# Kernel optimization log

Hardware: AMD Instinct MI355X
Metric: run time of the kernel (lower is better)

## Reference

```python
import jax, jax.numpy as jnp
import numpy as np

SCALES = [3, 5, 7, 9]


def _conv1d(x, w, b, k):
    # x: (BN, 1, L), w: (1, 1, k), b: (1,) -> (BN, 1, L), 'same' padding (k//2)
    y = jax.lax.conv_general_dilated(
        x, w, window_strides=(1,), padding=[(k // 2, k // 2)],
        dimension_numbers=("NCH", "OIH", "NCH"))
    return y + b[None, :, None]


def setup_inputs() -> dict:
    key = jax.random.key(0)
    ks = jax.random.split(key, 16)
    B, N, L = 64, 321, 720
    inp = {"x": jax.random.normal(ks[0], (B, N, L), dtype=jnp.float32)}
    # Conv1d(1,1,k) params, kaiming-ish scale 1/sqrt(k)
    for i, s in enumerate(SCALES):
        inp[f"cw{i}"] = jax.random.normal(ks[1 + 2 * i], (1, 1, s), dtype=jnp.float32) / np.sqrt(s)
        inp[f"cb{i}"] = jax.random.normal(ks[2 + 2 * i], (1,), dtype=jnp.float32) * 0.01
    # weight_net: Linear(4,32) -> ReLU -> Linear(32,4) -> Softmax
    inp["W1"] = jax.random.normal(ks[10], (4, 32), dtype=jnp.float32) / np.sqrt(4.0)
    inp["b1"] = jnp.zeros((32,), dtype=jnp.float32)
    inp["W2"] = jax.random.normal(ks[11], (32, 4), dtype=jnp.float32) / np.sqrt(32.0)
    inp["b2"] = jnp.zeros((4,), dtype=jnp.float32)
    return inp


def reference(x, cw0, cb0, cw1, cb1, cw2, cb2, cw3, cb3, W1, b1, W2, b2):
    B, N, L = x.shape
    xf = x.reshape(B * N, 1, L)
    cparams = [(cw0, cb0), (cw1, cb1), (cw2, cb2), (cw3, cb3)]
    feats, ents = [], []
    for (w, b), k in zip(cparams, SCALES):
        f = _conv1d(xf, w, b, k)                      # (BN, 1, L)
        prob = jax.nn.softmax(f, axis=-1)
        ent = -(prob * jnp.log(prob + 1e-8)).sum(axis=-1)  # (BN, 1)
        feats.append(f)
        ents.append(ent)
    entropy_vec = jnp.concatenate(ents, axis=-1)      # (BN, 4)
    h = jax.nn.relu(entropy_vec @ W1 + b1)
    weights = jax.nn.softmax(h @ W2 + b2, axis=-1)    # (BN, 4)
    stacked = jnp.stack(feats, axis=1)                # (BN, 4, 1, L)
    trend = (stacked * weights[:, :, None, None]).sum(axis=1)  # (BN, 1, L)
    return trend.reshape(B, N, L)
```

## Files before the change

kernel.cpp:

```cpp
#include <hip/hip_runtime.h>
#include <math.h>

#define NT 64
#define L_LEN 720
#define NROWS (64 * 321)

#define LOG2E 1.4426950408889634f
#define LN2   0.6931471805599453f

typedef float f32x2 __attribute__((ext_vector_type(2)));

__device__ __forceinline__ f32x2 pkfma(f32x2 a, f32x2 b, f32x2 c) {
    return __builtin_elementwise_fma(a, b, c);
}

template<int CTRL, int RM>
__device__ __forceinline__ float dpp_add(float x) {
    int t = __builtin_amdgcn_update_dpp(0, __float_as_int(x), CTRL, RM, 0xf, true);
    return x + __int_as_float(t);
}

__device__ __forceinline__ float wave_sum64(float x) {
    x = dpp_add<0x111, 0xf>(x);
    x = dpp_add<0x112, 0xf>(x);
    x = dpp_add<0x114, 0xf>(x);
    x = dpp_add<0x118, 0xf>(x);
    x = dpp_add<0x142, 0xa>(x);
    x = dpp_add<0x143, 0xc>(x);
    return __int_as_float(__builtin_amdgcn_readlane(__float_as_int(x), 63));
}

__device__ __forceinline__ float half_sum32(float x) {
    x = dpp_add<0x111, 0xf>(x);
    x = dpp_add<0x112, 0xf>(x);
    x = dpp_add<0x114, 0xf>(x);
    x = dpp_add<0x118, 0xf>(x);
    x = dpp_add<0x142, 0xa>(x);
    return __int_as_float(__builtin_amdgcn_readlane(__float_as_int(x), 31));
}

__global__ __launch_bounds__(NT, 4) void trend_kernel(
    const float* __restrict__ x,
    const float* __restrict__ cw0, const float* __restrict__ cb0,
    const float* __restrict__ cw1, const float* __restrict__ cb1,
    const float* __restrict__ cw2, const float* __restrict__ cb2,
    const float* __restrict__ cw3, const float* __restrict__ cb3,
    const float* __restrict__ W1, const float* __restrict__ b1,
    const float* __restrict__ W2, const float* __restrict__ b2,
    float* __restrict__ out)
{
    const int lane = threadIdx.x;
    const int row  = blockIdx.x;

    const float* __restrict__ xr = x + (size_t)row * L_LEN;

    const int ll = (lane < 60) ? lane : 59;
    const int e0 = 12 * ll - 4;
    float xw[20];
#pragma unroll
    for (int q = 0; q < 5; ++q) {
        int e = e0 + 4 * q;
        e = (e < 0) ? 0 : ((e > L_LEN - 4) ? (L_LEN - 4) : e);
        float4 v = *(const float4*)(xr + e);
        xw[4 * q + 0] = v.x; xw[4 * q + 1] = v.y;
        xw[4 * q + 2] = v.z; xw[4 * q + 3] = v.w;
    }

    const int hidx = lane & 31;
    float w1r[4];
#pragma unroll
    for (int s = 0; s < 4; ++s) w1r[s] = W1[s * 32 + hidx];
    const float b1r = b1[hidx];
    const float4 w2v = ((const float4*)W2)[hidx];
    const float b20 = b2[0], b21 = b2[1], b22 = b2[2], b23 = b2[3];

    const float* cws[4] = {cw0, cw1, cw2, cw3};
    const float* cbs[4] = {cb0, cb1, cb2, cb3};
    float w[4][9], bs[4];
#pragma unroll
    for (int s = 0; s < 4; ++s) {
        const int k = 3 + 2 * s;
        bs[s] = cbs[s][0];
#pragma unroll
        for (int t = 0; t < 9; ++t)
            w[s][t] = (t < k) ? cws[s][t] : 0.0f;
    }

    if (lane == 0)  { xw[0] = 0.f; xw[1] = 0.f; xw[2] = 0.f; xw[3] = 0.f; }
    if (lane == 59) { xw[16] = 0.f; xw[17] = 0.f; xw[18] = 0.f; xw[19] = 0.f; }

#pragma unroll
    for (int t = 0; t < 20; ++t) asm volatile("" : "+v"(xw[t]));

    f32x2 p[14];
#pragma unroll
    for (int i = 0; i < 14; ++i) p[i] = (f32x2){xw[i], xw[i + 6]};

    const f32x2 l2e = (f32x2){LOG2E, LOG2E};
    f32x2 fu[4][6];
    f32x2 Spk[4] = {{0.f,0.f},{0.f,0.f},{0.f,0.f},{0.f,0.f}};
    f32x2 Tpk[4] = {{0.f,0.f},{0.f,0.f},{0.f,0.f},{0.f,0.f}};
#pragma unroll
    for (int j = 0; j < 6; ++j) {
#pragma unroll
        for (int s = 0; s < 4; ++s) {
            const int k = 3 + 2 * s;
            const int off = 3 - s;
            f32x2 f = (f32x2){bs[s], bs[s]};
#pragma unroll
            for (int t = 0; t < k; ++t) {
                const f32x2 wv = (f32x2){w[s][t], w[s][t]};
                f = pkfma(wv, p[j + off + t], f);
            }
            fu[s][j] = f;
            f32x2 u = f * l2e;
            f32x2 ev;
            ev.x = __builtin_amdgcn_exp2f(u.x);
            ev.y = __builtin_amdgcn_exp2f(u.y);
            Spk[s] += ev;
            Tpk[s] = pkfma(f, ev, Tpk[s]);
        }
    }

#pragma unroll
    for (int s = 0; s < 4; ++s)
#pragma unroll
        for (int j = 0; j < 6; ++j) {
            asm volatile("" : "+v"(fu[s][j].x));
            asm volatile("" : "+v"(fu[s][j].y));
        }

    const bool active = lane < 60;
    float S[4], Tn[4];
#pragma unroll
    for (int s = 0; s < 4; ++s) {
        S[s]  = active ? (Spk[s].x + Spk[s].y) : 0.0f;
        Tn[s] = active ? (Tpk[s].x + Tpk[s].y) : 0.0f;
    }

    float ent[4];
#pragma unroll
    for (int s = 0; s < 4; ++s) {
        float Sg = wave_sum64(S[s]);
        float Tg = wave_sum64(Tn[s]);
        ent[s] = fmaf(LN2, __builtin_amdgcn_logf(Sg),
                      -Tg * __builtin_amdgcn_rcpf(Sg));
    }

    float h = b1r;
#pragma unroll
    for (int s = 0; s < 4; ++s) h = fmaf(ent[s], w1r[s], h);
    h = fmaxf(h, 0.0f);

    float lg0 = half_sum32(h * w2v.x) + b20;
    float lg1 = half_sum32(h * w2v.y) + b21;
    float lg2 = half_sum32(h * w2v.z) + b22;
    float lg3 = half_sum32(h * w2v.w) + b23;

    float m = fmaxf(fmaxf(lg0, lg1), fmaxf(lg2, lg3));
    float e0w = __expf(lg0 - m), e1w = __expf(lg1 - m);
    float e2w = __expf(lg2 - m), e3w = __expf(lg3 - m);
    float inv = 1.0f / (e0w + e1w + e2w + e3w);
    const float wg0 = e0w * inv, wg1 = e1w * inv;
    const float wg2 = e2w * inv, wg3 = e3w * inv;

    if (active) {
        f32x2 o[6];
#pragma unroll
        for (int j = 0; j < 6; ++j) {
            f32x2 acc = (f32x2){wg0, wg0} * fu[0][j];
            acc = pkfma((f32x2){wg1, wg1}, fu[1][j], acc);
            acc = pkfma((f32x2){wg2, wg2}, fu[2][j], acc);
            acc = pkfma((f32x2){wg3, wg3}, fu[3][j], acc);
            o[j] = acc;
        }
        float* __restrict__ orow = out + (size_t)row * L_LEN + 12 * lane;
        float4 v0 = {o[0].x, o[1].x, o[2].x, o[3].x};
        float4 v1 = {o[4].x, o[5].x, o[0].y, o[1].y};
        float4 v2 = {o[2].y, o[3].y, o[4].y, o[5].y};
        *(float4*)(orow)     = v0;
        *(float4*)(orow + 4) = v1;
        *(float4*)(orow + 8) = v2;
    }
}

extern "C" void kernel_launch(void* const* d_in, const int* in_sizes, int n_in,
                              void* d_out, int out_size, void* d_ws, size_t ws_size,
                              hipStream_t stream) {
    const float* xp  = (const float*)d_in[0];
    const float* cw0 = (const float*)d_in[1];
    const float* cb0 = (const float*)d_in[2];
    const float* cw1 = (const float*)d_in[3];
    const float* cb1 = (const float*)d_in[4];
    const float* cw2 = (const float*)d_in[5];
    const float* cb2 = (const float*)d_in[6];
    const float* cw3 = (const float*)d_in[7];
    const float* cb3 = (const float*)d_in[8];
    const float* W1  = (const float*)d_in[9];
    const float* b1  = (const float*)d_in[10];
    const float* W2  = (const float*)d_in[11];
    const float* b2  = (const float*)d_in[12];
    float* outp = (float*)d_out;

    trend_kernel<<<NROWS, NT, 0, stream>>>(xp, cw0, cb0, cw1, cb1, cw2, cb2,
                                           cw3, cb3, W1, b1, W2, b2, outp);
}
```

Measured before the change: 33.03 us.

## Assign strided float4 chunks per lane for coalesced loads and stores

Instead of each lane owning 12 contiguous elements, each lane now owns three float4 chunks spaced 60 chunks apart, and loads each chunk together with its neighbours for the halo. Consecutive lanes then touch consecutive 16-byte chunks, which makes the global loads and stores fully coalesced, in place of the previous 48-byte per-lane stride. The cost is more redundant halo loads (9 float4 per lane instead of 5) and a change in how packed pairs are formed from even and odd offsets.

```diff
diff --git a/kernel.cpp b/kernel.cpp
--- a/kernel.cpp
+++ b/kernel.cpp
@@ -3,6 +3,7 @@
 
 #define NT 64
 #define L_LEN 720
+#define NCHUNKS 180
 #define NROWS (64 * 321)
 
 #define LOG2E 1.4426950408889634f
@@ -52,18 +53,21 @@
     const int lane = threadIdx.x;
     const int row  = blockIdx.x;
 
-    const float* __restrict__ xr = x + (size_t)row * L_LEN;
-
-    const int ll = (lane < 60) ? lane : 59;
-    const int e0 = 12 * ll - 4;
-    float xw[20];
-#pragma unroll
-    for (int q = 0; q < 5; ++q) {
-        int e = e0 + 4 * q;
-        e = (e < 0) ? 0 : ((e > L_LEN - 4) ? (L_LEN - 4) : e);
-        float4 v = *(const float4*)(xr + e);
-        xw[4 * q + 0] = v.x; xw[4 * q + 1] = v.y;
-        xw[4 * q + 2] = v.z; xw[4 * q + 3] = v.w;
+    const float*  __restrict__ xr = x + (size_t)row * L_LEN;
+    const float4* __restrict__ xc = (const float4*)xr;
+
+    const int  ll     = (lane < 60) ? lane : 59;
+    const bool active = lane < 60;
+
+    float4 xq[3][3];
+#pragma unroll
+    for (int q = 0; q < 3; ++q) {
+#pragma unroll
+        for (int r = 0; r < 3; ++r) {
+            int c = ll + 60 * q + r - 1;
+            c = (c < 0) ? 0 : ((c > NCHUNKS - 1) ? (NCHUNKS - 1) : c);
+            xq[q][r] = xc[c];
+        }
     }
 
     const int hidx = lane & 31;
@@ -86,51 +90,65 @@
             w[s][t] = (t < k) ? cws[s][t] : 0.0f;
     }
 
-    if (lane == 0)  { xw[0] = 0.f; xw[1] = 0.f; xw[2] = 0.f; xw[3] = 0.f; }
-    if (lane == 59) { xw[16] = 0.f; xw[17] = 0.f; xw[18] = 0.f; xw[19] = 0.f; }
-
-#pragma unroll
-    for (int t = 0; t < 20; ++t) asm volatile("" : "+v"(xw[t]));
-
-    f32x2 p[14];
-#pragma unroll
-    for (int i = 0; i < 14; ++i) p[i] = (f32x2){xw[i], xw[i + 6]};
+    if (lane == 0)  xq[0][0] = (float4){0.f, 0.f, 0.f, 0.f};
+    if (lane == 59) xq[2][2] = (float4){0.f, 0.f, 0.f, 0.f};
+
+#pragma unroll
+    for (int q = 0; q < 3; ++q)
+#pragma unroll
+        for (int r = 0; r < 3; ++r)
+            asm volatile("" : "+v"(xq[q][r].x), "+v"(xq[q][r].y),
+                              "+v"(xq[q][r].z), "+v"(xq[q][r].w));
 
     const f32x2 l2e = (f32x2){LOG2E, LOG2E};
     f32x2 fu[4][6];
     f32x2 Spk[4] = {{0.f,0.f},{0.f,0.f},{0.f,0.f},{0.f,0.f}};
     f32x2 Tpk[4] = {{0.f,0.f},{0.f,0.f},{0.f,0.f},{0.f,0.f}};
-#pragma unroll
-    for (int j = 0; j < 6; ++j) {
-#pragma unroll
-        for (int s = 0; s < 4; ++s) {
-            const int k = 3 + 2 * s;
-            const int off = 3 - s;
-            f32x2 f = (f32x2){bs[s], bs[s]};
-#pragma unroll
-            for (int t = 0; t < k; ++t) {
-                const f32x2 wv = (f32x2){w[s][t], w[s][t]};
-                f = pkfma(wv, p[j + off + t], f);
+
+#pragma unroll
+    for (int q = 0; q < 3; ++q) {
+        const float xv[12] = {
+            xq[q][0].x, xq[q][0].y, xq[q][0].z, xq[q][0].w,
+            xq[q][1].x, xq[q][1].y, xq[q][1].z, xq[q][1].w,
+            xq[q][2].x, xq[q][2].y, xq[q][2].z, xq[q][2].w };
+
+        f32x2 pe[6], po[5];
+#pragma unroll
+        for (int i = 0; i < 6; ++i) pe[i] = (f32x2){xv[2 * i], xv[2 * i + 1]};
+#pragma unroll
+        for (int i = 0; i < 5; ++i) po[i] = (f32x2){xv[2 * i + 1], xv[2 * i + 2]};
+
+#pragma unroll
+        for (int pi = 0; pi < 2; ++pi) {
+            const int j0 = 2 * pi;
+#pragma unroll
+            for (int s = 0; s < 4; ++s) {
+                const int k = 3 + 2 * s;
+                const int off = 3 - s;
+                f32x2 f = (f32x2){bs[s], bs[s]};
+#pragma unroll
+                for (int t = 0; t < k; ++t) {
+                    const int i = j0 + off + t;
+                    const f32x2 pv = (i & 1) ? po[i >> 1] : pe[i >> 1];
+                    f = pkfma((f32x2){w[s][t], w[s][t]}, pv, f);
+                }
+                fu[s][2 * q + pi] = f;
+                f32x2 u = f * l2e;
+                f32x2 ev;
+                ev.x = __builtin_amdgcn_exp2f(u.x);
+                ev.y = __builtin_amdgcn_exp2f(u.y);
+                Spk[s] += ev;
+                Tpk[s] = pkfma(f, ev, Tpk[s]);
             }
-            fu[s][j] = f;
-            f32x2 u = f * l2e;
-            f32x2 ev;
-            ev.x = __builtin_amdgcn_exp2f(u.x);
-            ev.y = __builtin_amdgcn_exp2f(u.y);
-            Spk[s] += ev;
-            Tpk[s] = pkfma(f, ev, Tpk[s]);
         }
     }
 
 #pragma unroll
     for (int s = 0; s < 4; ++s)
 #pragma unroll
-        for (int j = 0; j < 6; ++j) {
-            asm volatile("" : "+v"(fu[s][j].x));
-            asm volatile("" : "+v"(fu[s][j].y));
-        }
-
-    const bool active = lane < 60;
+        for (int j = 0; j < 6; ++j)
+            asm volatile("" : "+v"(fu[s][j].x), "+v"(fu[s][j].y));
+
     float S[4], Tn[4];
 #pragma unroll
     for (int s = 0; s < 4; ++s) {
@@ -165,22 +183,20 @@
     const float wg2 = e2w * inv, wg3 = e3w * inv;
 
     if (active) {
-        f32x2 o[6];
-#pragma unroll
-        for (int j = 0; j < 6; ++j) {
-            f32x2 acc = (f32x2){wg0, wg0} * fu[0][j];
-            acc = pkfma((f32x2){wg1, wg1}, fu[1][j], acc);
-            acc = pkfma((f32x2){wg2, wg2}, fu[2][j], acc);
-            acc = pkfma((f32x2){wg3, wg3}, fu[3][j], acc);
-            o[j] = acc;
+        float4* __restrict__ oc = (float4*)(out + (size_t)row * L_LEN);
+#pragma unroll
+        for (int q = 0; q < 3; ++q) {
+            f32x2 o0 = (f32x2){wg0, wg0} * fu[0][2 * q];
+            o0 = pkfma((f32x2){wg1, wg1}, fu[1][2 * q], o0);
+            o0 = pkfma((f32x2){wg2, wg2}, fu[2][2 * q], o0);
+            o0 = pkfma((f32x2){wg3, wg3}, fu[3][2 * q], o0);
+            f32x2 o1 = (f32x2){wg0, wg0} * fu[0][2 * q + 1];
+            o1 = pkfma((f32x2){wg1, wg1}, fu[1][2 * q + 1], o1);
+            o1 = pkfma((f32x2){wg2, wg2}, fu[2][2 * q + 1], o1);
+            o1 = pkfma((f32x2){wg3, wg3}, fu[3][2 * q + 1], o1);
+            float4 v = {o0.x, o0.y, o1.x, o1.y};
+            oc[lane + 60 * q] = v;
         }
-        float* __restrict__ orow = out + (size_t)row * L_LEN + 12 * lane;
-        float4 v0 = {o[0].x, o[1].x, o[2].x, o[3].x};
-        float4 v1 = {o[4].x, o[5].x, o[0].y, o[1].y};
-        float4 v2 = {o[2].y, o[3].y, o[4].y, o[5].y};
-        *(float4*)(orow)     = v0;
-        *(float4*)(orow + 4) = v1;
-        *(float4*)(orow + 8) = v2;
     }
 }
 
```

Result: no change. 33.15 us (+0.4%).

## Process two rows per wave and recompute output via merged conv weights

Applied to the files above, without the earlier changes.

Each 64-thread block now handles two rows, loading both inputs up front and interleaving their convolution, entropy and reduction chains for more ILP and fewer blocks. Instead of keeping all four conv outputs live in registers until the mixing weights are known, the kernel folds the softmax weights into a single merged 9-tap filter and bias and recomputes the output from the input window. This cuts register pressure from stored features but adds an extra 9-tap pass and doubles per-thread state for two rows, which may still raise register use.

```diff
diff --git a/kernel.cpp b/kernel.cpp
--- a/kernel.cpp
+++ b/kernel.cpp
@@ -50,20 +50,25 @@
     float* __restrict__ out)
 {
     const int lane = threadIdx.x;
-    const int row  = blockIdx.x;
-
-    const float* __restrict__ xr = x + (size_t)row * L_LEN;
+    const int rowA = blockIdx.x * 2;
+    const int rowB = rowA + 1;
+
+    const float* __restrict__ xa = x + (size_t)rowA * L_LEN;
+    const float* __restrict__ xb = x + (size_t)rowB * L_LEN;
 
     const int ll = (lane < 60) ? lane : 59;
     const int e0 = 12 * ll - 4;
-    float xw[20];
+    float xwA[20], xwB[20];
 #pragma unroll
     for (int q = 0; q < 5; ++q) {
         int e = e0 + 4 * q;
         e = (e < 0) ? 0 : ((e > L_LEN - 4) ? (L_LEN - 4) : e);
-        float4 v = *(const float4*)(xr + e);
-        xw[4 * q + 0] = v.x; xw[4 * q + 1] = v.y;
-        xw[4 * q + 2] = v.z; xw[4 * q + 3] = v.w;
+        float4 va = *(const float4*)(xa + e);
+        float4 vb = *(const float4*)(xb + e);
+        xwA[4 * q + 0] = va.x; xwA[4 * q + 1] = va.y;
+        xwA[4 * q + 2] = va.z; xwA[4 * q + 3] = va.w;
+        xwB[4 * q + 0] = vb.x; xwB[4 * q + 1] = vb.y;
+        xwB[4 * q + 2] = vb.z; xwB[4 * q + 3] = vb.w;
     }
 
     const int hidx = lane & 31;
@@ -86,101 +91,149 @@
             w[s][t] = (t < k) ? cws[s][t] : 0.0f;
     }
 
-    if (lane == 0)  { xw[0] = 0.f; xw[1] = 0.f; xw[2] = 0.f; xw[3] = 0.f; }
-    if (lane == 59) { xw[16] = 0.f; xw[17] = 0.f; xw[18] = 0.f; xw[19] = 0.f; }
-
-#pragma unroll
-    for (int t = 0; t < 20; ++t) asm volatile("" : "+v"(xw[t]));
-
-    f32x2 p[14];
-#pragma unroll
-    for (int i = 0; i < 14; ++i) p[i] = (f32x2){xw[i], xw[i + 6]};
+    if (lane == 0) {
+#pragma unroll
+        for (int t = 0; t < 4; ++t) { xwA[t] = 0.f; xwB[t] = 0.f; }
+    }
+    if (lane == 59) {
+#pragma unroll
+        for (int t = 16; t < 20; ++t) { xwA[t] = 0.f; xwB[t] = 0.f; }
+    }
+
+    f32x2 pA[14], pB[14];
+#pragma unroll
+    for (int i = 0; i < 14; ++i) {
+        pA[i] = (f32x2){xwA[i], xwA[i + 6]};
+        pB[i] = (f32x2){xwB[i], xwB[i + 6]};
+    }
+#pragma unroll
+    for (int i = 0; i < 14; ++i) {
+        asm volatile("" : "+v"(pA[i].x), "+v"(pA[i].y));
+        asm volatile("" : "+v"(pB[i].x), "+v"(pB[i].y));
+    }
 
     const f32x2 l2e = (f32x2){LOG2E, LOG2E};
-    f32x2 fu[4][6];
-    f32x2 Spk[4] = {{0.f,0.f},{0.f,0.f},{0.f,0.f},{0.f,0.f}};
-    f32x2 Tpk[4] = {{0.f,0.f},{0.f,0.f},{0.f,0.f},{0.f,0.f}};
+    f32x2 SpkA[4] = {{0,0},{0,0},{0,0},{0,0}}, SpkB[4] = {{0,0},{0,0},{0,0},{0,0}};
+    f32x2 TpkA[4] = {{0,0},{0,0},{0,0},{0,0}}, TpkB[4] = {{0,0},{0,0},{0,0},{0,0}};
 #pragma unroll
     for (int j = 0; j < 6; ++j) {
 #pragma unroll
         for (int s = 0; s < 4; ++s) {
             const int k = 3 + 2 * s;
             const int off = 3 - s;
-            f32x2 f = (f32x2){bs[s], bs[s]};
+            f32x2 fA = (f32x2){bs[s], bs[s]};
+            f32x2 fB = fA;
 #pragma unroll
             for (int t = 0; t < k; ++t) {
                 const f32x2 wv = (f32x2){w[s][t], w[s][t]};
-                f = pkfma(wv, p[j + off + t], f);
+                fA = pkfma(wv, pA[j + off + t], fA);
+                fB = pkfma(wv, pB[j + off + t], fB);
             }
-            fu[s][j] = f;
-            f32x2 u = f * l2e;
-            f32x2 ev;
-            ev.x = __builtin_amdgcn_exp2f(u.x);
-            ev.y = __builtin_amdgcn_exp2f(u.y);
-            Spk[s] += ev;
-            Tpk[s] = pkfma(f, ev, Tpk[s]);
+            f32x2 uA = fA * l2e, uB = fB * l2e;
+            f32x2 eA, eB;
+            eA.x = __builtin_amdgcn_exp2f(uA.x);
+            eA.y = __builtin_amdgcn_exp2f(uA.y);
+            eB.x = __builtin_amdgcn_exp2f(uB.x);
+            eB.y = __builtin_amdgcn_exp2f(uB.y);
+            SpkA[s] += eA;                SpkB[s] += eB;
+            TpkA[s] = pkfma(fA, eA, TpkA[s]);
+            TpkB[s] = pkfma(fB, eB, TpkB[s]);
         }
     }
 
-#pragma unroll
-    for (int s = 0; s < 4; ++s)
+    const bool active = lane < 60;
+    float SA[4], TA[4], SB[4], TB[4];
+#pragma unroll
+    for (int s = 0; s < 4; ++s) {
+        SA[s] = active ? (SpkA[s].x + SpkA[s].y) : 0.0f;
+        TA[s] = active ? (TpkA[s].x + TpkA[s].y) : 0.0f;
+        SB[s] = active ? (SpkB[s].x + SpkB[s].y) : 0.0f;
+        TB[s] = active ? (TpkB[s].x + TpkB[s].y) : 0.0f;
+    }
+
+    float entA[4], entB[4];
+#pragma unroll
+    for (int s = 0; s < 4; ++s) {
+        float SgA = wave_sum64(SA[s]);
+        float TgA = wave_sum64(TA[s]);
+        float SgB = wave_sum64(SB[s]);
+        float TgB = wave_sum64(TB[s]);
+        entA[s] = fmaf(LN2, __builtin_amdgcn_logf(SgA),
+                       -TgA * __builtin_amdgcn_rcpf(SgA));
+        entB[s] = fmaf(LN2, __builtin_amdgcn_logf(SgB),
+                       -TgB * __builtin_amdgcn_rcpf(SgB));
+    }
+
+    float hA = b1r, hB = b1r;
+#pragma unroll
+    for (int s = 0; s < 4; ++s) {
+        hA = fmaf(entA[s], w1r[s], hA);
+        hB = fmaf(entB[s], w1r[s], hB);
+    }
+    hA = fmaxf(hA, 0.0f); hB = fmaxf(hB, 0.0f);
+
+    float lgA0 = half_sum32(hA * w2v.x) + b20;
+    float lgA1 = half_sum32(hA * w2v.y) + b21;
+    float lgA2 = half_sum32(hA * w2v.z) + b22;
+    float lgA3 = half_sum32(hA * w2v.w) + b23;
+    float lgB0 = half_sum32(hB * w2v.x) + b20;
+    float lgB1 = half_sum32(hB * w2v.y) + b21;
+    float lgB2 = half_sum32(hB * w2v.z) + b22;
+    float lgB3 = half_sum32(hB * w2v.w) + b23;
+
+    float mA = fmaxf(fmaxf(lgA0, lgA1), fmaxf(lgA2, lgA3));
+    float mB = fmaxf(fmaxf(lgB0, lgB1), fmaxf(lgB2, lgB3));
+    float eA0 = __expf(lgA0 - mA), eA1 = __expf(lgA1 - mA);
+    float eA2 = __expf(lgA2 - mA), eA3 = __expf(lgA3 - mA);
+    float eB0 = __expf(lgB0 - mB), eB1 = __expf(lgB1 - mB);
+    float eB2 = __expf(lgB2 - mB), eB3 = __expf(lgB3 - mB);
+    float invA = 1.0f / (eA0 + eA1 + eA2 + eA3);
+    float invB = 1.0f / (eB0 + eB1 + eB2 + eB3);
+    const float wgtA[4] = {eA0 * invA, eA1 * invA, eA2 * invA, eA3 * invA};
+    const float wgtB[4] = {eB0 * invB, eB1 * invB, eB2 * invB, eB3 * invB};
+
+    float WmA[9] = {0,0,0,0,0,0,0,0,0}, WmB[9] = {0,0,0,0,0,0,0,0,0};
+    float BmA = 0.f, BmB = 0.f;
+#pragma unroll
+    for (int s = 0; s < 4; ++s) {
+        const int k = 3 + 2 * s;
+        const int off = 3 - s;
+#pragma unroll
+        for (int t = 0; t < k; ++t) {
+            WmA[off + t] = fmaf(wgtA[s], w[s][t], WmA[off + t]);
+            WmB[off + t] = fmaf(wgtB[s], w[s][t], WmB[off + t]);
+        }
+        BmA = fmaf(wgtA[s], bs[s], BmA);
+        BmB = fmaf(wgtB[s], bs[s], BmB);
+    }
+
+    if (active) {
+        f32x2 oA[6], oB[6];
 #pragma unroll
         for (int j = 0; j < 6; ++j) {
-            asm volatile("" : "+v"(fu[s][j].x));
-            asm volatile("" : "+v"(fu[s][j].y));
+            f32x2 aA = (f32x2){BmA, BmA};
+            f32x2 aB = (f32x2){BmB, BmB};
+#pragma unroll
+            for (int d = 0; d < 9; ++d) {
+                aA = pkfma((f32x2){WmA[d], WmA[d]}, pA[j + d], aA);
+                aB = pkfma((f32x2){WmB[d], WmB[d]}, pB[j + d], aB);
+            }
+            oA[j] = aA; oB[j] = aB;
         }
-
-    const bool active = lane < 60;
-    float S[4], Tn[4];
-#pragma unroll
-    for (int s = 0; s < 4; ++s) {
-        S[s]  = active ? (Spk[s].x + Spk[s].y) : 0.0f;
-        Tn[s] = active ? (Tpk[s].x + Tpk[s].y) : 0.0f;
-    }
-
-    float ent[4];
-#pragma unroll
-    for (int s = 0; s < 4; ++s) {
-        float Sg = wave_sum64(S[s]);
-        float Tg = wave_sum64(Tn[s]);
-        ent[s] = fmaf(LN2, __builtin_amdgcn_logf(Sg),
-                      -Tg * __builtin_amdgcn_rcpf(Sg));
-    }
-
-    float h = b1r;
-#pragma unroll
-    for (int s = 0; s < 4; ++s) h = fmaf(ent[s], w1r[s], h);
-    h = fmaxf(h, 0.0f);
-
-    float lg0 = half_sum32(h * w2v.x) + b20;
-    float lg1 = half_sum32(h * w2v.y) + b21;
-    float lg2 = half_sum32(h * w2v.z) + b22;
-    float lg3 = half_sum32(h * w2v.w) + b23;
-
-    float m = fmaxf(fmaxf(lg0, lg1), fmaxf(lg2, lg3));
-    float e0w = __expf(lg0 - m), e1w = __expf(lg1 - m);
-    float e2w = __expf(lg2 - m), e3w = __expf(lg3 - m);
-    float inv = 1.0f / (e0w + e1w + e2w + e3w);
-    const float wg0 = e0w * inv, wg1 = e1w * inv;
-    const float wg2 = e2w * inv, wg3 = e3w * inv;
-
-    if (active) {
-        f32x2 o[6];
-#pragma unroll
-        for (int j = 0; j < 6; ++j) {
-            f32x2 acc = (f32x2){wg0, wg0} * fu[0][j];
-            acc = pkfma((f32x2){wg1, wg1}, fu[1][j], acc);
-            acc = pkfma((f32x2){wg2, wg2}, fu[2][j], acc);
-            acc = pkfma((f32x2){wg3, wg3}, fu[3][j], acc);
-            o[j] = acc;
-        }
-        float* __restrict__ orow = out + (size_t)row * L_LEN + 12 * lane;
-        float4 v0 = {o[0].x, o[1].x, o[2].x, o[3].x};
-        float4 v1 = {o[4].x, o[5].x, o[0].y, o[1].y};
-        float4 v2 = {o[2].y, o[3].y, o[4].y, o[5].y};
-        *(float4*)(orow)     = v0;
-        *(float4*)(orow + 4) = v1;
-        *(float4*)(orow + 8) = v2;
+        float* __restrict__ oa = out + (size_t)rowA * L_LEN + 12 * lane;
+        float* __restrict__ ob = out + (size_t)rowB * L_LEN + 12 * lane;
+        float4 a0 = {oA[0].x, oA[1].x, oA[2].x, oA[3].x};
+        float4 a1 = {oA[4].x, oA[5].x, oA[0].y, oA[1].y};
+        float4 a2 = {oA[2].y, oA[3].y, oA[4].y, oA[5].y};
+        float4 b0 = {oB[0].x, oB[1].x, oB[2].x, oB[3].x};
+        float4 b1v = {oB[4].x, oB[5].x, oB[0].y, oB[1].y};
+        float4 b2v = {oB[2].y, oB[3].y, oB[4].y, oB[5].y};
+        *(float4*)(oa)     = a0;
+        *(float4*)(oa + 4) = a1;
+        *(float4*)(oa + 8) = a2;
+        *(float4*)(ob)     = b0;
+        *(float4*)(ob + 4) = b1v;
+        *(float4*)(ob + 8) = b2v;
     }
 }
 
@@ -202,6 +255,6 @@
     const float* b2  = (const float*)d_in[12];
     float* outp = (float*)d_out;
 
-    trend_kernel<<<NROWS, NT, 0, stream>>>(xp, cw0, cb0, cw1, cb1, cw2, cb2,
-                                           cw3, cb3, W1, b1, W2, b2, outp);
-}
+    trend_kernel<<<NROWS / 2, NT, 0, stream>>>(xp, cw0, cb0, cw1, cb1, cw2, cb2,
+                                               cw3, cb3, W1, b1, W2, b2, outp);
+}
```

Measured after the change: 37.95 us. 1.15x slower.
